# Kernel optimization log

Measured on AMD Instinct MI355X. Metric: run time of the kernel, lower is better.

## Reference

```python
import jax, jax.numpy as jnp
import numpy as np

B, L, H = 8, 4096, 1024


def setup_inputs() -> dict:
    key = jax.random.key(0)
    k1, k2 = jax.random.split(key)
    sequence_output = jax.random.normal(k1, (B, L, H), dtype=jnp.float32)
    # each wordpiece position maps to the token it belongs to (monotone non-decreasing)
    wordpiece_to_token = jnp.sort(
        jax.random.randint(k2, (B, L), 0, L, dtype=jnp.int32), axis=-1
    )
    return {"sequence_output": sequence_output, "wordpiece_to_token": wordpiece_to_token}


def reference(sequence_output, wordpiece_to_token):
    # output[b, t, :] = sum over wordpieces w with wordpiece_to_token[b, w] == t
    b_, l_, h_ = sequence_output.shape
    # offset segment ids per batch element so one flat segment_sum handles all
    seg = (wordpiece_to_token.astype(jnp.int32) + jnp.arange(b_, dtype=jnp.int32)[:, None] * l_)
    out = jax.ops.segment_sum(
        sequence_output.reshape(b_ * l_, h_), seg.reshape(-1), num_segments=b_ * l_
    )
    return out.reshape(b_, l_, h_)
```

## Files before the change

kernel.cpp:

```cpp
#include <hip/hip_runtime.h>


#define B_DIM 8
#define L_DIM 4096
#define H_DIM 1024
#define LSTRIDE (L_DIM + 8)
#define TPW 4

__global__ __launch_bounds__(256) void build_starts_kernel(
    const int* __restrict__ tok,
    int* __restrict__ start)
{
    const int gid = blockIdx.x * 256 + threadIdx.x;
    const int b = gid >> 12;
    const int w = gid & (L_DIM - 1);

    const int* __restrict__ row = tok + (size_t)b * L_DIM;
    const int cur  = row[w];
    const int prev = (w > 0) ? row[w - 1] : -1;

    int* __restrict__ srow = start + (size_t)b * LSTRIDE;
    for (int t = prev + 1; t <= cur; ++t) srow[t] = w;
    if (w == L_DIM - 1) {
        for (int t = cur + 1; t <= L_DIM; ++t) srow[t] = L_DIM;
    }
}

__device__ __forceinline__ void acc4(float4& a, const float4 v) {
    a.x += v.x; a.y += v.y; a.z += v.z; a.w += v.w;
}

__global__ __launch_bounds__(256) void token_seg_sum_kernel(
    const float* __restrict__ seq,
    const int* __restrict__ start,
    float* __restrict__ out)
{
    const int wid   = (blockIdx.x << 2) | (threadIdx.x >> 6);
    const int lane  = threadIdx.x & 63;
    const int tglob = wid * TPW;
    const int b     = tglob >> 12;
    const int t0    = tglob & (L_DIM - 1);

    const int* __restrict__ srow = start + b * LSTRIDE + t0;
    int st[TPW + 1];
#pragma unroll
    for (int i = 0; i <= TPW; ++i) st[i] = srow[i];

    const float4* __restrict__ base  = (const float4*)seq + ((size_t)b << 20);
    float4* __restrict__       obase = (float4*)out + ((size_t)tglob << 8);

#pragma unroll
    for (int i = 0; i < TPW; ++i) {
        float4 a0 = make_float4(0.f, 0.f, 0.f, 0.f);
        float4 a1 = a0, a2 = a0, a3 = a0;

        const int s = st[i];
        const int e = st[i + 1];
        for (int w = s; w < e; ++w) {
            const float4* __restrict__ r = base + ((size_t)w << 8) + lane;
            float4 v0 = r[0];
            float4 v1 = r[64];
            float4 v2 = r[128];
            float4 v3 = r[192];
            acc4(a0, v0); acc4(a1, v1); acc4(a2, v2); acc4(a3, v3);
        }

        float4* __restrict__ o = obase + (i << 8) + lane;
        o[0]   = a0;
        o[64]  = a1;
        o[128] = a2;
        o[192] = a3;
    }
}

extern "C" void kernel_launch(void* const* d_in, const int* in_sizes, int n_in,
                              void* d_out, int out_size, void* d_ws, size_t ws_size,
                              hipStream_t stream) {
    const float* seq = (const float*)d_in[0];
    const int*   tok = (const int*)d_in[1];
    float*       out = (float*)d_out;
    int*         start = (int*)d_ws;

    build_starts_kernel<<<dim3(B_DIM * L_DIM / 256), dim3(256), 0, stream>>>(tok, start);

    token_seg_sum_kernel<<<dim3(B_DIM * L_DIM / (TPW * 4)), dim3(256), 0, stream>>>(
        seq, start, out);
}
```

Measured before the change: 243.5 us.

## Halve tokens per wave, unroll wordpiece loop by two, use nontemporal output stores

Each wave now handles two tokens instead of four, which doubles the grid and spreads the irregular per-token work across more waves. The wordpiece accumulation loop is unrolled by two so eight 16-byte loads are in flight per iteration, with a remainder step for odd counts. Output writes switch to nontemporal stores through ext_vector_type to keep the write-only result from occupying cache. The unroll raises register use, and the smaller per-wave work adds launch and index overhead.

```diff
diff --git a/kernel.cpp b/kernel.cpp
--- a/kernel.cpp
+++ b/kernel.cpp
@@ -5,7 +5,9 @@
 #define L_DIM 4096
 #define H_DIM 1024
 #define LSTRIDE (L_DIM + 8)
-#define TPW 4
+#define TPW 2
+
+typedef float fx4 __attribute__((ext_vector_type(4)));
 
 __global__ __launch_bounds__(256) void build_starts_kernel(
     const int* __restrict__ tok,
@@ -26,7 +28,7 @@
     }
 }
 
-__device__ __forceinline__ void acc4(float4& a, const float4 v) {
+__device__ __forceinline__ void acc4(fx4& a, const float4 v) {
     a.x += v.x; a.y += v.y; a.z += v.z; a.w += v.w;
 }
 
@@ -47,29 +49,44 @@
     for (int i = 0; i <= TPW; ++i) st[i] = srow[i];
 
     const float4* __restrict__ base  = (const float4*)seq + ((size_t)b << 20);
-    float4* __restrict__       obase = (float4*)out + ((size_t)tglob << 8);
+    fx4* __restrict__          obase = (fx4*)out + ((size_t)tglob << 8);
 
 #pragma unroll
     for (int i = 0; i < TPW; ++i) {
-        float4 a0 = make_float4(0.f, 0.f, 0.f, 0.f);
-        float4 a1 = a0, a2 = a0, a3 = a0;
+        fx4 a0 = (fx4)0.f;
+        fx4 a1 = a0, a2 = a0, a3 = a0;
 
         const int s = st[i];
         const int e = st[i + 1];
-        for (int w = s; w < e; ++w) {
-            const float4* __restrict__ r = base + ((size_t)w << 8) + lane;
-            float4 v0 = r[0];
-            float4 v1 = r[64];
-            float4 v2 = r[128];
-            float4 v3 = r[192];
+        int w = s;
+        for (; w + 2 <= e; w += 2) {
+            const float4* __restrict__ r0 = base + ((size_t)w << 8) + lane;
+            const float4* __restrict__ r1 = r0 + 256;
+            float4 v0 = r0[0];
+            float4 v1 = r0[64];
+            float4 v2 = r0[128];
+            float4 v3 = r0[192];
+            float4 u0 = r1[0];
+            float4 u1 = r1[64];
+            float4 u2 = r1[128];
+            float4 u3 = r1[192];
+            acc4(a0, v0); acc4(a1, v1); acc4(a2, v2); acc4(a3, v3);
+            acc4(a0, u0); acc4(a1, u1); acc4(a2, u2); acc4(a3, u3);
+        }
+        if (w < e) {
+            const float4* __restrict__ r0 = base + ((size_t)w << 8) + lane;
+            float4 v0 = r0[0];
+            float4 v1 = r0[64];
+            float4 v2 = r0[128];
+            float4 v3 = r0[192];
             acc4(a0, v0); acc4(a1, v1); acc4(a2, v2); acc4(a3, v3);
         }
 
-        float4* __restrict__ o = obase + (i << 8) + lane;
-        o[0]   = a0;
-        o[64]  = a1;
-        o[128] = a2;
-        o[192] = a3;
+        fx4* __restrict__ o = obase + (i << 8) + lane;
+        __builtin_nontemporal_store(a0, o);
+        __builtin_nontemporal_store(a1, o + 64);
+        __builtin_nontemporal_store(a2, o + 128);
+        __builtin_nontemporal_store(a3, o + 192);
     }
 }
 
```

New measurement: 238.6 us. -2.0%, faster.
